# Kernel optimization log

Measured on AMD Instinct MI355X. Metric: run time of the kernel, lower is better.

The kernel has to match this reference:

```python
import jax, jax.numpy as jnp
import numpy as np

B, N, F, T, O, K = 4, 4000, 16, 16, 16, 3
LN_EPS = 1e-5


def setup_inputs() -> dict:
    key = jax.random.key(0)
    k = jax.random.split(key, 18)
    rn = lambda i, sh, sc=1.0: jax.random.normal(k[i], sh, dtype=jnp.float32) * np.float32(sc)
    ru = lambda i, sh: jax.random.uniform(k[i], sh, dtype=jnp.float32)
    return {
        "x": rn(0, (B, N, F, T)),
        # scale the random Laplacian so the Chebyshev recurrence stays numerically sane
        "laplacian": rn(1, (N, N), 1.0 / np.sqrt(N)),
        "W1": ru(2, (T,)),
        "W2": rn(3, (F, T)),
        "W3": ru(4, (F,)),
        "bs": ru(5, (1, N, N)),
        "Vs": ru(6, (N, N)),
        "U1": ru(7, (N,)),
        "U2": rn(8, (F, N)),
        "U3": ru(9, (F,)),
        "be": ru(10, (1, T, T)),
        "Ve": ru(11, (T, T)),
        "cheb_w": rn(12, (K, F, O), 1.0 / np.sqrt(F)),
        "time_w": rn(13, (O, F, T), 1.0 / np.sqrt(F * T)),
        "time_b": rn(14, (O,)),
        "ln_g": jnp.ones((N, O), dtype=jnp.float32),
        "ln_b": jnp.zeros((N, O), dtype=jnp.float32),
    }


def reference(x, laplacian, W1, W2, W3, bs, Vs, U1, U2, U3, be, Ve,
              cheb_w, time_w, time_b, ln_g, ln_b):
    # ---- temporal attention: E (B,T,T) ----
    # lhs[b,t] = sum_{n,f} x[b,n,f,t] * U1[n]
    t_lhs = jnp.einsum('bnft,n->bt', x, U1)
    # rhs[b,t] = sum_{n,f,g} x[b,n,f,t] * U2[g,n] * U3[g]
    t_rhs = jnp.einsum('bnft,gn,g->bt', x, U2, U3)
    t_prod = t_lhs[:, :, None] * t_rhs[:, None, :]          # (B,T,T) outer product
    E = jnp.einsum('ts,bsr->btr', Ve, jax.nn.sigmoid(t_prod + be))
    E = jax.nn.softmax(E, axis=-1)

    # apply temporal attention along the time axis: (B,N,F,T)
    x_TAt = jnp.einsum('bts,bnfs->bnft', E, x)

    # ---- spatial attention: S (B,N,N) ----
    s_lhs = jnp.einsum('bnft,t->bnf', x, W1)                 # (B,N,F)
    # faithful to the source ops (valid since F == T here)
    s_rhs = jnp.einsum('bnkt,gk,t->bng', x, W2, W3)          # (B,N,F)
    s_prod = jnp.einsum('bnf,bmf->bnm', s_lhs, s_rhs)        # (B,N,N)
    S = jnp.einsum('nm,bmk->bnk', Vs, jax.nn.sigmoid(s_prod + bs))
    S = jax.nn.softmax(S, axis=-1)

    # spatially attended features for all timesteps at once
    x_SAtt = jnp.einsum('bnm,bmft->bnft', S, x_TAt)          # (B,N,F,T)

    # ---- Chebyshev graph conv over every timestep ----
    Tx0 = x_SAtt
    out = jnp.einsum('bnft,fo->bnot', Tx0, cheb_w[0])
    Tx1 = jnp.einsum('nm,bmft->bnft', laplacian, Tx0)
    out = out + jnp.einsum('bnft,fo->bnot', Tx1, cheb_w[1])
    for kk in range(2, K):
        Tx2 = 2.0 * jnp.einsum('nm,bmft->bnft', laplacian, Tx1) - Tx0
        out = out + jnp.einsum('bnft,fo->bnot', Tx2, cheb_w[kk])
        Tx0, Tx1 = Tx1, Tx2
    spatial_gcn_avg = out.mean(axis=-1)                      # (B,N,O)

    # ---- time conv: Conv2d(in,out,kernel=(1,T)) == full contraction over (F,T) ----
    time_out = jnp.einsum('bnct,oct->bno', x, time_w) + time_b

    # ---- residual (in_channels == out_channels branch) ----
    residual = x[:, :, :, -1]                                # (B,N,O)

    y = spatial_gcn_avg + time_out + residual
    # LayerNorm over the last two dims [N, O]
    mean = y.mean(axis=(1, 2), keepdims=True)
    var = jnp.var(y, axis=(1, 2), keepdims=True)
    y = (y - mean) / jnp.sqrt(var + LN_EPS) * ln_g + ln_b
    return jax.nn.relu(y)
```

## Files before the change

### kernel.cpp

```cpp
#include <hip/hip_runtime.h>
#include <math.h>

#define Bc 4
#define Nn 4000
#define KS 4096
#define NP (16000000 + 4096)

typedef _Float16 half8 __attribute__((ext_vector_type(8)));
typedef float f32x4 __attribute__((ext_vector_type(4)));
typedef unsigned short u16x4 __attribute__((ext_vector_type(4)));

static __device__ __forceinline__ unsigned short f2h(float f) {
  _Float16 h = (_Float16)f;
  unsigned short u;
  __builtin_memcpy(&u, &h, 2);
  return u;
}
static __device__ __forceinline__ float h2f(unsigned short u) {
  _Float16 h;
  __builtin_memcpy(&h, &u, 2);
  return (float)h;
}
static __device__ __forceinline__ void gld16(const void* g, void* l) {
  __builtin_amdgcn_global_load_lds(
      (const __attribute__((address_space(1))) unsigned int*)g,
      (__attribute__((address_space(3))) unsigned int*)l, 16, 0, 0);
}

__global__ __launch_bounds__(256) void k1_trhs(
    const float* __restrict__ x, const float* __restrict__ U1,
    const float* __restrict__ U2, const float* __restrict__ U3,
    float* __restrict__ tl, float* __restrict__ tr) {
  int b = blockIdx.y;
  int tid = threadIdx.x;
  int q = tid & 3;
  int n = blockIdx.x * 64 + (tid >> 2);
  float xs[16];
#pragma unroll
  for (int t = 0; t < 16; ++t) xs[t] = 0.f;
  float c1 = 0.f, c2 = 0.f;
  if (n < Nn) {
    const float* xr = x + ((size_t)b * Nn + n) * 256 + q * 64;
#pragma unroll
    for (int f = 0; f < 4; ++f) {
#pragma unroll
      for (int qq = 0; qq < 4; ++qq) {
        float4 v = *(const float4*)(xr + f * 16 + qq * 4);
        xs[qq * 4 + 0] += v.x; xs[qq * 4 + 1] += v.y;
        xs[qq * 4 + 2] += v.z; xs[qq * 4 + 3] += v.w;
      }
    }
    c1 = U1[n];
#pragma unroll
    for (int g = 0; g < 4; ++g) {
      int gg = q * 4 + g;
      c2 += U2[(size_t)gg * Nn + n] * U3[gg];
    }
  }
#pragma unroll
  for (int m = 1; m < 4; m <<= 1) {
    c2 += __shfl_xor(c2, m, 64);
#pragma unroll
    for (int t = 0; t < 16; ++t) xs[t] += __shfl_xor(xs[t], m, 64);
  }
  float v1[4], v2[4];
#pragma unroll
  for (int i = 0; i < 4; ++i) {
    int t = q * 4 + i;
    v1[i] = c1 * xs[t];
    v2[i] = c2 * xs[t];
  }
#pragma unroll
  for (int off = 4; off < 64; off <<= 1) {
#pragma unroll
    for (int i = 0; i < 4; ++i) {
      v1[i] += __shfl_down(v1[i], off, 64);
      v2[i] += __shfl_down(v2[i], off, 64);
    }
  }
  int lane = tid & 63;
  if (lane < 4) {
#pragma unroll
    for (int i = 0; i < 4; ++i) {
      atomicAdd(&tl[b * 16 + lane * 4 + i], v1[i]);
      atomicAdd(&tr[b * 16 + lane * 4 + i], v2[i]);
    }
  }
}

__global__ __launch_bounds__(256) void k2_eattn(
    const float* __restrict__ tl, const float* __restrict__ tr,
    const float* __restrict__ be, const float* __restrict__ Ve,
    float* __restrict__ ecol) {
  int b = blockIdx.x;
  int tid = threadIdx.x;
  __shared__ float sig[256];
  __shared__ float Em[256];
  int s = tid >> 4, r = tid & 15;
  float z = tl[b * 16 + s] * tr[b * 16 + r] + be[s * 16 + r];
  sig[s * 16 + r] = 1.0f / (1.0f + __expf(-z));
  __syncthreads();
  float e = 0.f;
#pragma unroll
  for (int ss = 0; ss < 16; ++ss) e += Ve[s * 16 + ss] * sig[ss * 16 + r];
  Em[s * 16 + r] = e;
  __syncthreads();
  if (tid < 16) {
    float m = -1e30f;
#pragma unroll
    for (int rr = 0; rr < 16; ++rr) m = fmaxf(m, Em[tid * 16 + rr]);
    float ssum = 0.f;
    float ex[16];
#pragma unroll
    for (int rr = 0; rr < 16; ++rr) { ex[rr] = __expf(Em[tid * 16 + rr] - m); ssum += ex[rr]; }
    float inv = 1.0f / ssum;
#pragma unroll
    for (int rr = 0; rr < 16; ++rr) Em[tid * 16 + rr] = ex[rr] * inv;
  }
  __syncthreads();
  if (tid < 16) {
    float c = 0.f;
#pragma unroll
    for (int tt = 0; tt < 16; ++tt) c += Em[tt * 16 + tid];
    ecol[b * 16 + tid] = c;
  }
}

__global__ __launch_bounds__(256) void k3_pern(
    const float* __restrict__ x, const float* __restrict__ ecol,
    const float* __restrict__ W1, const float* __restrict__ W2,
    const float* __restrict__ W3, const float* __restrict__ time_w,
    const float* __restrict__ time_b,
    float* __restrict__ xts, float* __restrict__ slhs,
    float* __restrict__ srhs, float* __restrict__ base) {
  __shared__ float tws[4096];
  __shared__ float W1s[16], W3s[16], Ecs[16], tbs[16], W2s[256];
  int tid = threadIdx.x;
  int b = blockIdx.y;
  for (int i = tid; i < 4096; i += 256) tws[i] = time_w[i];
  W2s[tid] = W2[tid & 255];
  if (tid < 16) {
    W1s[tid] = W1[tid]; W3s[tid] = W3[tid];
    Ecs[tid] = ecol[b * 16 + tid]; tbs[tid] = time_b[tid];
  }
  __syncthreads();
  int n = blockIdx.x * 256 + tid;
  if (n >= Nn) return;
  const float* xr = x + ((size_t)b * Nn + n) * 256;
  float xtsv[16], slv[16], xw3[16], to[16], resid[16];
#pragma unroll
  for (int i = 0; i < 16; ++i) { xtsv[i] = 0; slv[i] = 0; xw3[i] = 0; to[i] = 0; }
  for (int f = 0; f < 16; ++f) {
    float xf[16];
#pragma unroll
    for (int q = 0; q < 4; ++q) {
      float4 v = *(const float4*)(xr + f * 16 + q * 4);
      xf[q * 4 + 0] = v.x; xf[q * 4 + 1] = v.y; xf[q * 4 + 2] = v.z; xf[q * 4 + 3] = v.w;
    }
    float a = 0, c = 0, d = 0;
#pragma unroll
    for (int t2 = 0; t2 < 16; ++t2) {
      a += Ecs[t2] * xf[t2];
      c += W1s[t2] * xf[t2];
      d += W3s[t2] * xf[t2];
    }
    xtsv[f] = a; slv[f] = c; xw3[f] = d; resid[f] = xf[15];
#pragma unroll
    for (int o = 0; o < 16; ++o) {
      float acc = 0;
#pragma unroll
      for (int t2 = 0; t2 < 16; ++t2) acc += tws[o * 256 + f * 16 + t2] * xf[t2];
      to[o] += acc;
    }
  }
  size_t o16 = ((size_t)b * Nn + n) * 16;
#pragma unroll
  for (int g = 0; g < 16; ++g) {
    float acc = 0;
#pragma unroll
    for (int k2 = 0; k2 < 16; ++k2) acc += W2s[g * 16 + k2] * xw3[k2];
    srhs[o16 + g] = acc;
  }
#pragma unroll
  for (int i = 0; i < 16; ++i) {
    xts[o16 + i] = xtsv[i];
    slhs[o16 + i] = slv[i];
    base[o16 + i] = to[i] + tbs[i] + resid[i];
  }
}

__global__ __launch_bounds__(256) void fconv(
    const float* __restrict__ src, unsigned short* __restrict__ dst) {
  size_t i = ((size_t)blockIdx.x * 256 + threadIdx.x) * 4;
  float4 v = *(const float4*)(src + i);
  u16x4 h;
  h.x = f2h(v.x); h.y = f2h(v.y); h.z = f2h(v.z); h.w = f2h(v.w);
  *(u16x4*)(dst + i) = h;
}

__global__ __launch_bounds__(256) void vconv2(
    const float* __restrict__ Vs, unsigned short* __restrict__ Vh) {
  int row = blockIdx.y;
  int col = blockIdx.x * 1024 + threadIdx.x * 4;
  u16x4 h;
  if (row < Nn && col < Nn) {
    float4 v = *(const float4*)(Vs + (size_t)row * Nn + col);
    h.x = f2h(v.x); h.y = f2h(v.y); h.z = f2h(v.z); h.w = f2h(v.w);
  } else {
    h.x = 0; h.y = 0; h.z = 0; h.w = 0;
  }
  *(u16x4*)(Vh + (size_t)row * KS + col) = h;
}

__global__ __launch_bounds__(256) void tsconv(
    const float* __restrict__ ts, unsigned short* __restrict__ tsT) {
  int n = blockIdx.x * 256 + threadIdx.x;
  int col = blockIdx.y;
  if (n >= Nn) return;
  int b = col >> 4, f = col & 15;
  tsT[(size_t)col * Nn + n] = f2h(ts[((size_t)b * Nn + n) * 16 + f]);
}

__global__ __launch_bounds__(256) void gemm1_P(
    const float* __restrict__ slhs, const float* __restrict__ srhs,
    const unsigned short* __restrict__ bsH, unsigned short* __restrict__ PhT, int b) {
  __shared__ float Ms[64][17];
  __shared__ float Cs[64][17];
  __shared__ float Pt[64][65];
  int tid = threadIdx.x;
  int m0 = blockIdx.y * 64, k0 = blockIdx.x * 64;
  int lr = tid >> 2, lq = (tid & 3) << 2;
  {
    int gm = m0 + lr; if (gm > Nn - 1) gm = Nn - 1;
    float4 v = *(const float4*)(slhs + ((size_t)b * Nn + gm) * 16 + lq);
    Ms[lr][lq + 0] = v.x; Ms[lr][lq + 1] = v.y; Ms[lr][lq + 2] = v.z; Ms[lr][lq + 3] = v.w;
    int gk = k0 + lr; if (gk > Nn - 1) gk = Nn - 1;
    float4 w = *(const float4*)(srhs + ((size_t)b * Nn + gk) * 16 + lq);
    Cs[lr][lq + 0] = w.x; Cs[lr][lq + 1] = w.y; Cs[lr][lq + 2] = w.z; Cs[lr][lq + 3] = w.w;
  }
  __syncthreads();
  int tx = tid & 15, ty = tid >> 4;
  float acc[4][4] = {};
#pragma unroll
  for (int f = 0; f < 16; ++f) {
    float a4[4], b4[4];
#pragma unroll
    for (int i = 0; i < 4; ++i) a4[i] = Ms[ty * 4 + i][f];
#pragma unroll
    for (int j = 0; j < 4; ++j) b4[j] = Cs[tx * 4 + j][f];
#pragma unroll
    for (int i = 0; i < 4; ++i)
#pragma unroll
      for (int j = 0; j < 4; ++j) acc[i][j] += a4[i] * b4[j];
  }
#pragma unroll
  for (int i = 0; i < 4; ++i) {
    int m = m0 + ty * 4 + i;
    int k = k0 + tx * 4;
    float bv[4] = {0.f, 0.f, 0.f, 0.f};
    if (m < Nn) {
      if (k + 3 < Nn) {
        u16x4 t4 = *(const u16x4*)(bsH + (size_t)m * Nn + k);
        bv[0] = h2f(t4.x); bv[1] = h2f(t4.y); bv[2] = h2f(t4.z); bv[3] = h2f(t4.w);
      } else {
        for (int j = 0; j < 4; ++j)
          if (k + j < Nn) bv[j] = h2f(bsH[(size_t)m * Nn + k + j]);
      }
    }
#pragma unroll
    for (int j = 0; j < 4; ++j) {
      float z = acc[i][j] + bv[j];
      Pt[ty * 4 + i][tx * 4 + j] = 1.f / (1.f + __expf(-z));
    }
  }
  __syncthreads();
#pragma unroll
  for (int i = 0; i < 4; ++i) {
    int kl = ty * 4 + i;
    int ml = tx * 4;
    int gm = m0 + ml;
    u16x4 h;
    h.x = f2h(Pt[ml + 0][kl]);
    h.y = f2h(Pt[ml + 1][kl]);
    h.z = f2h(Pt[ml + 2][kl]);
    h.w = f2h(Pt[ml + 3][kl]);
    size_t off = (size_t)(k0 + kl) * KS + gm;
    if (gm + 3 < Nn) {
      *(u16x4*)(PhT + off) = h;
    } else {
      unsigned short hv[4] = {h.x, h.y, h.z, h.w};
      for (int q = 0; q < 4; ++q)
        if (gm + q < Nn) PhT[off + q] = hv[q];
    }
  }
}

__global__ __launch_bounds__(512, 2) void gemm2_mfma(
    const unsigned short* __restrict__ Vh, const unsigned short* __restrict__ PhT,
    float* __restrict__ SP, unsigned int* __restrict__ rmaxu) {
  __shared__ unsigned short Ah[2][2][8192];
  __shared__ unsigned short Bh[2][2][8192];
  int t = threadIdx.x;
  int bid = blockIdx.x;
  int wg = (bid & 7) * 32 + (bid >> 3);
  int row0 = (wg >> 4) * 256, col0 = (wg & 15) * 256;

  int sr = t >> 2, sg = t & 3;
  int ssw = sg ^ ((t >> 4) & 3);
  size_t a0 = (size_t)(row0 + sr) * KS + ssw * 8;
  size_t a1 = (size_t)(row0 + 128 + sr) * KS + ssw * 8;
  size_t b0 = (size_t)(col0 + sr) * KS + ssw * 8;
  size_t b1 = (size_t)(col0 + 128 + sr) * KS + ssw * 8;
  int ld0 = t * 8, ld1 = 4096 + t * 8;

  int lane = t & 63, wid = t >> 6;
  int wm = (wid >> 2) * 128, wn = (wid & 3) * 64;
  int ml = lane & 15, qd = lane >> 4;
  int gr = qd ^ ((ml >> 2) & 3);
  int aro[8], bro[4];
#pragma unroll
  for (int i = 0; i < 8; ++i) aro[i] = (wm + ml + i * 16) * 32 + gr * 8;
#pragma unroll
  for (int j = 0; j < 4; ++j) bro[j] = (wn + ml + j * 16) * 32 + gr * 8;

  f32x4 acc[8][4] = {};

#define STG(P, X, bf, kh, o0, o1, kt)                          \
  do {                                                         \
    size_t c_ = (size_t)(kt) * 64 + (kh) * 32;                 \
    gld16(P + (o0) + c_, &X[bf][kh][ld0]);                     \
    gld16(P + (o1) + c_, &X[bf][kh][ld1]);                     \
  } while (0)

  STG(Vh, Ah, 0, 0, a0, a1, 0); STG(PhT, Bh, 0, 0, b0, b1, 0);
  STG(Vh, Ah, 0, 1, a0, a1, 0); STG(PhT, Bh, 0, 1, b0, b1, 0);
  STG(Vh, Ah, 1, 0, a0, a1, 1); STG(PhT, Bh, 1, 0, b0, b1, 1);
  STG(Vh, Ah, 1, 1, a0, a1, 1); STG(PhT, Bh, 1, 1, b0, b1, 1);
  asm volatile("s_waitcnt vmcnt(12)" ::: "memory");
  __builtin_amdgcn_s_barrier();

#define PH_MFMA_BEGIN()                                        \
  __builtin_amdgcn_s_barrier();                                \
  asm volatile("s_waitcnt lgkmcnt(0)" ::: "memory");           \
  __builtin_amdgcn_sched_barrier(0);                           \
  __builtin_amdgcn_s_setprio(1)

#pragma unroll 1
  for (int G = 0; G < 64; ++G) {
    int cb = G & 1, nb = cb ^ 1;
    int tn1 = (G + 1 < 64) ? G + 1 : 63;
    int tn2 = (G + 2 < 64) ? G + 2 : 63;
    half8 av[4], bv[4];
#pragma unroll
    for (int j = 0; j < 4; ++j) bv[j] = *(const half8*)&Bh[cb][0][bro[j]];
#pragma unroll
    for (int i = 0; i < 4; ++i) av[i] = *(const half8*)&Ah[cb][0][aro[i]];
    STG(Vh, Ah, nb, 1, a0, a1, tn1);
    PH_MFMA_BEGIN();
#pragma unroll
    for (int i = 0; i < 4; ++i)
#pragma unroll
      for (int j = 0; j < 4; ++j)
        acc[i][j] = __builtin_amdgcn_mfma_f32_16x16x32_f16(av[i], bv[j], acc[i][j], 0, 0, 0);
    __builtin_amdgcn_s_setprio(0);
    __builtin_amdgcn_s_barrier();
#pragma unroll
    for (int i = 0; i < 4; ++i) av[i] = *(const half8*)&Ah[cb][0][aro[4 + i]];
    STG(PhT, Bh, nb, 1, b0, b1, tn1);
    PH_MFMA_BEGIN();
#pragma unroll
    for (int i = 0; i < 4; ++i)
#pragma unroll
      for (int j = 0; j < 4; ++j)
        acc[4 + i][j] = __builtin_amdgcn_mfma_f32_16x16x32_f16(av[i], bv[j], acc[4 + i][j], 0, 0, 0);
    __builtin_amdgcn_s_setprio(0);
    asm volatile("s_waitcnt vmcnt(8)" ::: "memory");
    __builtin_amdgcn_s_barrier();
#pragma unroll
    for (int j = 0; j < 4; ++j) bv[j] = *(const half8*)&Bh[cb][1][bro[j]];
#pragma unroll
    for (int i = 0; i < 4; ++i) av[i] = *(const half8*)&Ah[cb][1][aro[i]];
    STG(Vh, Ah, cb, 0, a0, a1, tn2);
    PH_MFMA_BEGIN();
#pragma unroll
    for (int i = 0; i < 4; ++i)
#pragma unroll
      for (int j = 0; j < 4; ++j)
        acc[i][j] = __builtin_amdgcn_mfma_f32_16x16x32_f16(av[i], bv[j], acc[i][j], 0, 0, 0);
    __builtin_amdgcn_s_setprio(0);
    __builtin_amdgcn_s_barrier();
#pragma unroll
    for (int i = 0; i < 4; ++i) av[i] = *(const half8*)&Ah[cb][1][aro[4 + i]];
    STG(PhT, Bh, cb, 0, b0, b1, tn2);
    PH_MFMA_BEGIN();
#pragma unroll
    for (int i = 0; i < 4; ++i)
#pragma unroll
      for (int j = 0; j < 4; ++j)
        acc[4 + i][j] = __builtin_amdgcn_mfma_f32_16x16x32_f16(av[i], bv[j], acc[4 + i][j], 0, 0, 0);
    __builtin_amdgcn_s_setprio(0);
    asm volatile("s_waitcnt vmcnt(8)" ::: "memory");
    __builtin_amdgcn_s_barrier();
  }
#undef STG
#undef PH_MFMA_BEGIN

#pragma unroll
  for (int i = 0; i < 8; ++i) {
#pragma unroll
    for (int r = 0; r < 4; ++r) {
      int grow = row0 + wm + i * 16 + qd * 4 + r;
      if (grow >= Nn) continue;
      float rowmax = -3.0e38f;
#pragma unroll
      for (int j = 0; j < 4; ++j) {
        int gcol = col0 + wn + j * 16 + ml;
        if (gcol < Nn) {
          float v = acc[i][j][r];
          SP[(size_t)grow * Nn + gcol] = v;
          rowmax = fmaxf(rowmax, v);
        }
      }
#pragma unroll
      for (int mk = 1; mk < 16; mk <<= 1)
        rowmax = fmaxf(rowmax, __shfl_xor(rowmax, mk, 64));
      if (ml == 0) {
        unsigned u = __float_as_uint(rowmax);
        u = (u & 0x80000000u) ? ~u : (u | 0x80000000u);
        atomicMax(rmaxu + grow, u);
      }
    }
  }
}

__global__ __launch_bounds__(256) void txsum_sp(
    const float* __restrict__ SP, const float* __restrict__ xts,
    const unsigned int* __restrict__ rmaxu, float* __restrict__ lsum,
    float* __restrict__ ts0, int b) {
  __shared__ float Ws[16][65];
  __shared__ float Xs[64][17];
  int tid = threadIdx.x;
  int n0 = blockIdx.x * 16;
  int kbase = blockIdx.y * 1000, kend = kbase + 1000;
  int r = tid >> 4, f = tid & 15;
  int lq = f * 4;
  int xr = tid >> 2, xc = (tid & 3) << 2;
  const float* spr = SP + (size_t)(n0 + r) * Nn;
  unsigned u = rmaxu[n0 + r];
  u = (u & 0x80000000u) ? (u ^ 0x80000000u) : ~u;
  float rm = __uint_as_float(u);
  float acc = 0.f, lpart = 0.f;
  for (int k0 = kbase; k0 < kend; k0 += 64) {
    int gx = k0 + xr;
    if (gx < kend) {
      float4 v = *(const float4*)(xts + ((size_t)b * Nn + gx) * 16 + xc);
      Xs[xr][xc + 0] = v.x; Xs[xr][xc + 1] = v.y; Xs[xr][xc + 2] = v.z; Xs[xr][xc + 3] = v.w;
    } else {
      Xs[xr][xc + 0] = 0.f; Xs[xr][xc + 1] = 0.f; Xs[xr][xc + 2] = 0.f; Xs[xr][xc + 3] = 0.f;
    }
    int gk = k0 + lq;
    float4 v = *(const float4*)(spr + gk);
    float e0 = (gk + 0 < kend) ? __expf(v.x - rm) : 0.f;
    float e1 = (gk + 1 < kend) ? __expf(v.y - rm) : 0.f;
    float e2 = (gk + 2 < kend) ? __expf(v.z - rm) : 0.f;
    float e3 = (gk + 3 < kend) ? __expf(v.w - rm) : 0.f;
    Ws[r][lq + 0] = e0; Ws[r][lq + 1] = e1; Ws[r][lq + 2] = e2; Ws[r][lq + 3] = e3;
    lpart += e0 + e1 + e2 + e3;
    __syncthreads();
#pragma unroll
    for (int kk = 0; kk < 64; ++kk) acc += Ws[r][kk] * Xs[kk][f];
    __syncthreads();
  }
#pragma unroll
  for (int mk = 1; mk < 16; mk <<= 1) lpart += __shfl_xor(lpart, mk, 64);
  if (f == 0) atomicAdd(&lsum[n0 + r], lpart);
  atomicAdd(&ts0[((size_t)b * Nn + n0 + r) * 16 + f], acc);
}

__global__ __launch_bounds__(256) void nrm_k(
    float* __restrict__ ts0, const float* __restrict__ lsum) {
  int tid = threadIdx.x;
  int b = blockIdx.y;
  int n = blockIdx.x * 16 + (tid >> 4);
  size_t i = ((size_t)b * Nn + n) * 16 + (tid & 15);
  ts0[i] = ts0[i] / lsum[b * Nn + n];
}

__global__ __launch_bounds__(256) void chebm(
    const unsigned short* __restrict__ lapH, const unsigned short* __restrict__ tsT,
    float* __restrict__ Cout) {
  __shared__ unsigned short Ah[64 * 32];
  __shared__ unsigned short Bh[64 * 32];
  int t = threadIdx.x;
  int row0 = blockIdx.x * 64;
  int kc0 = blockIdx.y * 25 * 32;
  int kc1 = kc0 + 25 * 32;
  int arow = row0 + (t >> 2); if (arow > Nn - 1) arow = Nn - 1;
  size_t a_base = (size_t)arow * Nn + (t & 3) * 8;
  size_t b_base = (size_t)(t >> 2) * Nn + (t & 3) * 8;

  int lane = t & 63;
  int wid = t >> 6;
  int wm = (wid >> 1) * 32, wn = (wid & 1) * 32;
  int ml = lane & 15, qd = lane >> 4;
  int aoff = (wm + ml) * 32 + qd * 8;
  int boff = (wn + ml) * 32 + qd * 8;

  f32x4 acc[2][2] = {};

  for (int k0 = kc0; k0 < kc1; k0 += 32) {
    gld16(lapH + a_base + k0, &Ah[t * 8]);
    gld16(tsT + b_base + k0, &Bh[t * 8]);
    __syncthreads();
    half8 a_h[2], b_h[2];
#pragma unroll
    for (int i = 0; i < 2; ++i) a_h[i] = *(const half8*)&Ah[aoff + i * 512];
#pragma unroll
    for (int j = 0; j < 2; ++j) b_h[j] = *(const half8*)&Bh[boff + j * 512];
#pragma unroll
    for (int i = 0; i < 2; ++i)
#pragma unroll
      for (int j = 0; j < 2; ++j)
        acc[i][j] = __builtin_amdgcn_mfma_f32_16x16x32_f16(a_h[i], b_h[j], acc[i][j], 0, 0, 0);
    __syncthreads();
  }
#pragma unroll
  for (int i = 0; i < 2; ++i)
#pragma unroll
    for (int j = 0; j < 2; ++j) {
      int gcol = wn + j * 16 + ml;
      int b = gcol >> 4, f = gcol & 15;
#pragma unroll
      for (int r = 0; r < 4; ++r) {
        int grow = row0 + wm + i * 16 + qd * 4 + r;
        if (grow < Nn) {
          size_t idx = ((size_t)b * Nn + grow) * 16 + f;
          atomicAdd(&Cout[idx], acc[i][j][r]);
        }
      }
    }
}

__global__ __launch_bounds__(256) void ky_k(
    const float* __restrict__ ts0, const float* __restrict__ ts1,
    const float* __restrict__ ts2, const float* __restrict__ cw,
    const float* __restrict__ base, float* __restrict__ ybuf,
    float* __restrict__ lnacc) {
  __shared__ float T0[256], T1[256], T2[256], CW[768];
  __shared__ float rs[256], rq[256];
  int tid = threadIdx.x;
  int b = blockIdx.y;
  size_t base_i = ((size_t)b * Nn + blockIdx.x * 16) * 16;
  T0[tid] = ts0[base_i + tid];
  T1[tid] = ts1[base_i + tid];
  T2[tid] = ts2[base_i + tid];
  for (int i = tid; i < 768; i += 256) CW[i] = cw[i];
  __syncthreads();
  int r = tid >> 4, o = tid & 15;
  float acc = 0.f;
#pragma unroll
  for (int f2 = 0; f2 < 16; ++f2) {
    float c2 = CW[512 + f2 * 16 + o];
    acc += T0[r * 16 + f2] * (CW[f2 * 16 + o] - c2);
    acc += T1[r * 16 + f2] * CW[256 + f2 * 16 + o];
    acc += (2.0f * T2[r * 16 + f2]) * c2;
  }
  float y = acc * 0.0625f + base[base_i + tid];
  ybuf[base_i + tid] = y;
  rs[tid] = y; rq[tid] = y * y;
  __syncthreads();
  for (int s2 = 128; s2 > 0; s2 >>= 1) {
    if (tid < s2) { rs[tid] += rs[tid + s2]; rq[tid] += rq[tid + s2]; }
    __syncthreads();
  }
  if (tid == 0) {
    atomicAdd(&lnacc[b * 2 + 0], rs[0]);
    atomicAdd(&lnacc[b * 2 + 1], rq[0]);
  }
}

__global__ __launch_bounds__(256) void kln_k(
    const float* __restrict__ ybuf, const float* __restrict__ lnacc,
    const float* __restrict__ lg, const float* __restrict__ lb,
    float* __restrict__ outp) {
  int tid = threadIdx.x;
  int b = blockIdx.y;
  size_t i = ((size_t)b * Nn + blockIdx.x * 16) * 16 + tid;
  size_t nz = (size_t)blockIdx.x * 256 + tid;
  const float inv = 1.0f / 64000.0f;
  float s = lnacc[b * 2 + 0], q = lnacc[b * 2 + 1];
  float mean = s * inv;
  float var = q * inv - mean * mean;
  float rstd = rsqrtf(var + 1e-5f);
  float v = (ybuf[i] - mean) * rstd * lg[nz] + lb[nz];
  outp[i] = fmaxf(v, 0.f);
}

extern "C" void kernel_launch(void* const* d_in, const int* in_sizes, int n_in,
                              void* d_out, int out_size, void* d_ws, size_t ws_size,
                              hipStream_t stream) {
  const float* x   = (const float*)d_in[0];
  const float* lap = (const float*)d_in[1];
  const float* W1  = (const float*)d_in[2];
  const float* W2  = (const float*)d_in[3];
  const float* W3  = (const float*)d_in[4];
  const float* bs  = (const float*)d_in[5];
  const float* Vs  = (const float*)d_in[6];
  const float* U1  = (const float*)d_in[7];
  const float* U2  = (const float*)d_in[8];
  const float* U3  = (const float*)d_in[9];
  const float* be  = (const float*)d_in[10];
  const float* Ve  = (const float*)d_in[11];
  const float* cw  = (const float*)d_in[12];
  const float* tw  = (const float*)d_in[13];
  const float* tb  = (const float*)d_in[14];
  const float* lg  = (const float*)d_in[15];
  const float* lb  = (const float*)d_in[16];
  float* ws = (float*)d_ws;
  float* SP = ws;
  unsigned short* Vh   = (unsigned short*)(ws + (size_t)NP);
  unsigned short* PhT  = Vh + (size_t)KS * KS;
  unsigned short* lapH = PhT + (size_t)KS * KS;
  unsigned short* bsH  = lapH + (size_t)Nn * Nn;
  unsigned short* tsT  = bsH + (size_t)Nn * Nn;
  float* xts  = (float*)(tsT + 64 * Nn + 64);
  float* slhs = xts + 256000;
  float* srhs = slhs + 256000;
  float* base = srhs + 256000;
  float* ts0  = base + 256000;
  float* ts1  = ts0 + 256000;
  float* ts2  = ts1 + 256000;
  float* ybuf = ts2 + 256000;
  float* tl   = ybuf + 256000;
  float* tr   = tl + 64;
  float* ecol = tr + 64;
  unsigned int* rmaxu = (unsigned int*)(ecol + 64);
  float* lsum = (float*)(rmaxu + Bc * Nn);
  float* lnacc = lsum + Bc * Nn;

  hipMemsetAsync(tl, 0, 128 * sizeof(float), stream);
  hipMemsetAsync(lnacc, 0, 8 * sizeof(float), stream);
  hipMemsetAsync(ts0, 0, 256000 * sizeof(float), stream);
  hipMemsetAsync(ts1, 0, 256000 * sizeof(float), stream);
  hipMemsetAsync(ts2, 0, 256000 * sizeof(float), stream);
  hipMemsetAsync(rmaxu, 0, Bc * Nn * sizeof(unsigned int), stream);
  hipMemsetAsync(lsum, 0, Bc * Nn * sizeof(float), stream);

  k1_trhs<<<dim3(63, 4), 256, 0, stream>>>(x, U1, U2, U3, tl, tr);
  k2_eattn<<<dim3(4), 256, 0, stream>>>(tl, tr, be, Ve, ecol);
  k3_pern<<<dim3(16, 4), 256, 0, stream>>>(x, ecol, W1, W2, W3, tw, tb,
                                           xts, slhs, srhs, base);
  vconv2<<<dim3(4, 4096), 256, 0, stream>>>(Vs, Vh);
  fconv<<<dim3(15625), 256, 0, stream>>>(lap, lapH);
  fconv<<<dim3(15625), 256, 0, stream>>>(bs, bsH);
  for (int b = 0; b < 4; ++b) {
    gemm1_P<<<dim3(63, 63), 256, 0, stream>>>(slhs, srhs, bsH, PhT, b);
    gemm2_mfma<<<dim3(256), 512, 0, stream>>>(Vh, PhT, SP, rmaxu + b * Nn);
    txsum_sp<<<dim3(250, 4), 256, 0, stream>>>(SP, xts, rmaxu + b * Nn,
                                               lsum + b * Nn, ts0, b);
  }
  nrm_k<<<dim3(250, 4), 256, 0, stream>>>(ts0, lsum);
  tsconv<<<dim3(16, 64), 256, 0, stream>>>(ts0, tsT);
  chebm<<<dim3(63, 5), 256, 0, stream>>>(lapH, tsT, ts1);
  tsconv<<<dim3(16, 64), 256, 0, stream>>>(ts1, tsT);
  chebm<<<dim3(63, 5), 256, 0, stream>>>(lapH, tsT, ts2);
  ky_k<<<dim3(250, 4), 256, 0, stream>>>(ts0, ts1, ts2, cw, base, ybuf, lnacc);
  kln_k<<<dim3(250, 4), 256, 0, stream>>>(ybuf, lnacc, lg, lb, (float*)d_out);
}
```

Before: 1.252 ms.

## Software-pipeline LDS fragment reads ahead of MFMA phases in spatial GEMM

Restructures the main GEMM loop so the LDS reads of A/B fragments for the next MFMA phase are issued before the current phase's MFMAs, using separate register sets (pa1-pa4, pb01, pb23). This lets LDS read latency overlap MFMA execution instead of serialising before each phase. It adds extra barriers and raises register pressure, which could lower occupancy or spill.

```diff
diff --git a/kernel.cpp b/kernel.cpp
--- a/kernel.cpp
+++ b/kernel.cpp
@@ -324,6 +324,7 @@
   for (int j = 0; j < 4; ++j) bro[j] = (wn + ml + j * 16) * 32 + gr * 8;
 
   f32x4 acc[8][4] = {};
+  half8 pa1[4], pa2[4], pa3[4], pa4[4], pb01[4], pb23[4];
 
 #define STG(P, X, bf, kh, o0, o1, kt)                          \
   do {                                                         \
@@ -331,79 +332,91 @@
     gld16(P + (o0) + c_, &X[bf][kh][ld0]);                     \
     gld16(P + (o1) + c_, &X[bf][kh][ld1]);                     \
   } while (0)
+#define SCHB() __builtin_amdgcn_sched_barrier(0)
+#define LGKM0() asm volatile("s_waitcnt lgkmcnt(0)" ::: "memory")
+#define VM8()   asm volatile("s_waitcnt vmcnt(8)" ::: "memory")
+#define BARR()  __builtin_amdgcn_s_barrier()
 
   STG(Vh, Ah, 0, 0, a0, a1, 0); STG(PhT, Bh, 0, 0, b0, b1, 0);
   STG(Vh, Ah, 0, 1, a0, a1, 0); STG(PhT, Bh, 0, 1, b0, b1, 0);
   STG(Vh, Ah, 1, 0, a0, a1, 1); STG(PhT, Bh, 1, 0, b0, b1, 1);
   STG(Vh, Ah, 1, 1, a0, a1, 1); STG(PhT, Bh, 1, 1, b0, b1, 1);
   asm volatile("s_waitcnt vmcnt(12)" ::: "memory");
-  __builtin_amdgcn_s_barrier();
-
-#define PH_MFMA_BEGIN()                                        \
-  __builtin_amdgcn_s_barrier();                                \
-  asm volatile("s_waitcnt lgkmcnt(0)" ::: "memory");           \
-  __builtin_amdgcn_sched_barrier(0);                           \
-  __builtin_amdgcn_s_setprio(1)
+  BARR();
+#pragma unroll
+  for (int j = 0; j < 4; ++j) pb01[j] = *(const half8*)&Bh[0][0][bro[j]];
+#pragma unroll
+  for (int i = 0; i < 4; ++i) pa1[i] = *(const half8*)&Ah[0][0][aro[i]];
 
 #pragma unroll 1
   for (int G = 0; G < 64; ++G) {
     int cb = G & 1, nb = cb ^ 1;
     int tn1 = (G + 1 < 64) ? G + 1 : 63;
     int tn2 = (G + 2 < 64) ? G + 2 : 63;
-    half8 av[4], bv[4];
-#pragma unroll
-    for (int j = 0; j < 4; ++j) bv[j] = *(const half8*)&Bh[cb][0][bro[j]];
-#pragma unroll
-    for (int i = 0; i < 4; ++i) av[i] = *(const half8*)&Ah[cb][0][aro[i]];
     STG(Vh, Ah, nb, 1, a0, a1, tn1);
-    PH_MFMA_BEGIN();
+    BARR(); LGKM0(); SCHB();
+#pragma unroll
+    for (int i = 0; i < 4; ++i) pa2[i] = *(const half8*)&Ah[cb][0][aro[4 + i]];
+    SCHB();
+    __builtin_amdgcn_s_setprio(1);
 #pragma unroll
     for (int i = 0; i < 4; ++i)
 #pragma unroll
       for (int j = 0; j < 4; ++j)
-        acc[i][j] = __builtin_amdgcn_mfma_f32_16x16x32_f16(av[i], bv[j], acc[i][j], 0, 0, 0);
+        acc[i][j] = __builtin_amdgcn_mfma_f32_16x16x32_f16(pa1[i], pb01[j], acc[i][j], 0, 0, 0);
     __builtin_amdgcn_s_setprio(0);
-    __builtin_amdgcn_s_barrier();
-#pragma unroll
-    for (int i = 0; i < 4; ++i) av[i] = *(const half8*)&Ah[cb][0][aro[4 + i]];
+    BARR();
     STG(PhT, Bh, nb, 1, b0, b1, tn1);
-    PH_MFMA_BEGIN();
+    VM8();
+    BARR(); LGKM0(); SCHB();
+#pragma unroll
+    for (int j = 0; j < 4; ++j) pb23[j] = *(const half8*)&Bh[cb][1][bro[j]];
+#pragma unroll
+    for (int i = 0; i < 4; ++i) pa3[i] = *(const half8*)&Ah[cb][1][aro[i]];
+    SCHB();
+    __builtin_amdgcn_s_setprio(1);
 #pragma unroll
     for (int i = 0; i < 4; ++i)
 #pragma unroll
       for (int j = 0; j < 4; ++j)
-        acc[4 + i][j] = __builtin_amdgcn_mfma_f32_16x16x32_f16(av[i], bv[j], acc[4 + i][j], 0, 0, 0);
+        acc[4 + i][j] = __builtin_amdgcn_mfma_f32_16x16x32_f16(pa2[i], pb01[j], acc[4 + i][j], 0, 0, 0);
     __builtin_amdgcn_s_setprio(0);
-    asm volatile("s_waitcnt vmcnt(8)" ::: "memory");
-    __builtin_amdgcn_s_barrier();
-#pragma unroll
-    for (int j = 0; j < 4; ++j) bv[j] = *(const half8*)&Bh[cb][1][bro[j]];
-#pragma unroll
-    for (int i = 0; i < 4; ++i) av[i] = *(const half8*)&Ah[cb][1][aro[i]];
+    BARR();
     STG(Vh, Ah, cb, 0, a0, a1, tn2);
-    PH_MFMA_BEGIN();
+    BARR(); LGKM0(); SCHB();
+#pragma unroll
+    for (int i = 0; i < 4; ++i) pa4[i] = *(const half8*)&Ah[cb][1][aro[4 + i]];
+    SCHB();
+    __builtin_amdgcn_s_setprio(1);
 #pragma unroll
     for (int i = 0; i < 4; ++i)
 #pragma unroll
       for (int j = 0; j < 4; ++j)
-        acc[i][j] = __builtin_amdgcn_mfma_f32_16x16x32_f16(av[i], bv[j], acc[i][j], 0, 0, 0);
+        acc[i][j] = __builtin_amdgcn_mfma_f32_16x16x32_f16(pa3[i], pb23[j], acc[i][j], 0, 0, 0);
     __builtin_amdgcn_s_setprio(0);
-    __builtin_amdgcn_s_barrier();
-#pragma unroll
-    for (int i = 0; i < 4; ++i) av[i] = *(const half8*)&Ah[cb][1][aro[4 + i]];
+    BARR();
     STG(PhT, Bh, cb, 0, b0, b1, tn2);
-    PH_MFMA_BEGIN();
+    VM8();
+    BARR(); LGKM0(); SCHB();
+#pragma unroll
+    for (int j = 0; j < 4; ++j) pb01[j] = *(const half8*)&Bh[nb][0][bro[j]];
+#pragma unroll
+    for (int i = 0; i < 4; ++i) pa1[i] = *(const half8*)&Ah[nb][0][aro[i]];
+    SCHB();
+    __builtin_amdgcn_s_setprio(1);
 #pragma unroll
     for (int i = 0; i < 4; ++i)
 #pragma unroll
       for (int j = 0; j < 4; ++j)
-        acc[4 + i][j] = __builtin_amdgcn_mfma_f32_16x16x32_f16(av[i], bv[j], acc[4 + i][j], 0, 0, 0);
+        acc[4 + i][j] = __builtin_amdgcn_mfma_f32_16x16x32_f16(pa4[i], pb23[j], acc[4 + i][j], 0, 0, 0);
     __builtin_amdgcn_s_setprio(0);
-    asm volatile("s_waitcnt vmcnt(8)" ::: "memory");
-    __builtin_amdgcn_s_barrier();
+    BARR();
   }
 #undef STG
-#undef PH_MFMA_BEGIN
+#undef SCHB
+#undef LGKM0
+#undef VM8
+#undef BARR
 
 #pragma unroll
   for (int i = 0; i < 8; ++i) {
```

Result: slower. 1.309 ms (+4.5%).
